# Kernel tuning notes

Measured on AMD Instinct MI355X. Metric: run time of the kernel, lower is better.

The kernel has to match this reference:

```python
import jax, jax.numpy as jnp
import numpy as np

EMBED_DIM = 1024
NUM_HEADS = 4
HEAD_DIM = EMBED_DIM // NUM_HEADS  # 256
QKV_DIM = 64                        # NUM_HEADS * QKV_DIM == HEAD_DIM (required by the residual add)
B, S = 16, 4096


def setup_inputs() -> dict:
    key = jax.random.key(0)
    kx, kq, kk, kv = jax.random.split(key, 4)
    x = jax.random.normal(kx, (B, S, EMBED_DIM), dtype=jnp.float32)
    # torch nn.Linear weights have shape [out_features, in_features]; y = x @ W.T
    scale = 1.0 / np.sqrt(HEAD_DIM)
    W_q = jax.random.normal(kq, (QKV_DIM, HEAD_DIM), dtype=jnp.float32) * scale
    W_k = jax.random.normal(kk, (QKV_DIM, HEAD_DIM), dtype=jnp.float32) * scale
    W_v = jax.random.normal(kv, (QKV_DIM, HEAD_DIM), dtype=jnp.float32) * scale
    return {"x": x, "W_q": W_q, "W_k": W_k, "W_v": W_v}


def reference(x, W_q, W_k, W_v):
    b = x.shape[0]
    # [B, S, H, Dh] -> [B, H, S, Dh]
    xh = x.reshape(b, -1, NUM_HEADS, HEAD_DIM).transpose(0, 2, 1, 3)
    # Shared projections applied per head (vectorized over the head axis)
    Q = jnp.einsum('bhsd,qd->bhsq', xh, W_q)  # [B,H,S,Qk]
    K = jnp.einsum('bhsd,qd->bhsq', xh, W_k)
    V = jnp.einsum('bhsd,qd->bhsq', xh, W_v)
    # Nonstandard ordering from the original: scores = Q^T K over the sequence axis
    attn_scores = jnp.einsum('bhsq,bhsk->bhqk', Q, K) / np.sqrt(HEAD_DIM)  # [B,H,Qk,Qk]
    attn_weights = jax.nn.softmax(attn_scores, axis=-1)
    # attn_output is computed in the original but NOT used in the returned value
    attn_output = jnp.einsum('bhsq,bhqk->bhsk', V, attn_weights)  # dead code, DCE'd under jit
    del attn_output
    # cat(V per head, dim=-1) -> [B, S, H*Qk];  x_head is the LAST head's slice [B, S, Dh]
    V_cat = V.transpose(0, 2, 1, 3).reshape(b, -1, NUM_HEADS * QKV_DIM)
    x_last_head = xh[:, NUM_HEADS - 1]  # [B, S, Dh]
    return x_last_head + V_cat
```

## Files before the change

kernel.cpp:

```cpp
#include <hip/hip_runtime.h>
#include <hip/hip_bf16.h>


#define TOKENS_PER_BLOCK 128
#define NCHUNK 8
#define NBLOCKS (16 * 4096 / TOKENS_PER_BLOCK)

typedef short bf16x4 __attribute__((ext_vector_type(4)));
typedef short bf16x8 __attribute__((ext_vector_type(8)));
typedef float f32x4  __attribute__((ext_vector_type(4)));

__device__ __forceinline__ short f2bf(float f) {
    __hip_bfloat16 h = __float2bfloat16(f);
    return __builtin_bit_cast(short, h);
}
__device__ __forceinline__ bf16x4 cvt4(f32x4 a) {
    bf16x4 r;
    r[0] = f2bf(a[0]); r[1] = f2bf(a[1]); r[2] = f2bf(a[2]); r[3] = f2bf(a[3]);
    return r;
}
__device__ __forceinline__ bf16x8 cvt8(f32x4 a, f32x4 b) {
    bf16x8 r;
    r[0] = f2bf(a[0]); r[1] = f2bf(a[1]); r[2] = f2bf(a[2]); r[3] = f2bf(a[3]);
    r[4] = f2bf(b[0]); r[5] = f2bf(b[1]); r[6] = f2bf(b[2]); r[7] = f2bf(b[3]);
    return r;
}

__device__ __forceinline__ int xofs(int tok, int colbyte) {
    return tok * 2048 + (colbyte ^ ((tok & 7) << 4));
}

__global__ __launch_bounds__(256, 1) void mha_vcat_kernel(
    const float* __restrict__ x, const float* __restrict__ Wv,
    float* __restrict__ out)
{
    __shared__ char X[2][16 * 2048];

    const int tid  = threadIdx.x;
    const int wid  = tid >> 6;
    const int lane = tid & 63;
    const int cl   = lane & 15;
    const int g    = lane >> 4;

    const long blockTok = (long)blockIdx.x * TOKENS_PER_BLOCK;

    const int srow  = tid >> 7;
    const int scolA = (tid & 127) * 4;

    f32x4 sA[8], sB[8];
    #pragma unroll
    for (int p = 0; p < 8; ++p) {
        const float* q = x + (blockTok + p * 2 + srow) * 1024;
        sA[p] = *(const f32x4*)(q + scolA);
        sB[p] = *(const f32x4*)(q + 512 + scolA);
    }

    bf16x8 wfr[8][4];
    #pragma unroll
    for (int kk = 0; kk < 8; ++kk)
        #pragma unroll
        for (int n = 0; n < 4; ++n) {
            const float* q = Wv + (n * 16 + cl) * 256 + kk * 32 + g * 8;
            wfr[kk][n] = cvt8(*(const f32x4*)q, *(const f32x4*)(q + 4));
        }

    bf16x8 diag0, diag1;
    #pragma unroll
    for (int j = 0; j < 8; ++j) {
        diag0[j] = (g * 8 + j == cl)      ? f2bf(1.0f) : (short)0;
        diag1[j] = (g * 8 + j == cl + 16) ? f2bf(1.0f) : (short)0;
    }

    #pragma unroll
    for (int p = 0; p < 8; ++p) {
        const int lt = p * 2 + srow;
        *(bf16x4*)(&X[0][xofs(lt, scolA * 2)])        = cvt4(sA[p]);
        *(bf16x4*)(&X[0][xofs(lt, 1024 + scolA * 2)]) = cvt4(sB[p]);
    }
    __syncthreads();

    #pragma unroll
    for (int c = 0; c < NCHUNK; ++c) {
        if (c < NCHUNK - 1) {
            #pragma unroll
            for (int p = 0; p < 8; ++p) {
                const float* q = x + (blockTok + (c + 1) * 16 + p * 2 + srow) * 1024;
                sA[p] = *(const f32x4*)(q + scolA);
                sB[p] = *(const f32x4*)(q + 512 + scolA);
            }
        }

        const char* Xb = X[c & 1];
        f32x4 acc[4];
        #pragma unroll
        for (int n = 0; n < 4; ++n) acc[n] = (f32x4){0.f, 0.f, 0.f, 0.f};

        #pragma unroll
        for (int kk = 0; kk < 8; ++kk) {
            const bf16x8 xf = *(const bf16x8*)(
                Xb + xofs(cl, wid * 512 + kk * 64 + g * 16));
            #pragma unroll
            for (int n = 0; n < 4; ++n)
                acc[n] = __builtin_amdgcn_mfma_f32_16x16x32_bf16(
                    wfr[kk][n], xf, acc[n], 0, 0, 0);
        }
        #pragma unroll
        for (int s = 0; s < 2; ++s) {
            const bf16x8 x3 = *(const bf16x8*)(
                Xb + xofs(cl, 1536 + wid * 128 + s * 64 + g * 16));
            acc[2 * s]     = __builtin_amdgcn_mfma_f32_16x16x32_bf16(
                diag0, x3, acc[2 * s], 0, 0, 0);
            acc[2 * s + 1] = __builtin_amdgcn_mfma_f32_16x16x32_bf16(
                diag1, x3, acc[2 * s + 1], 0, 0, 0);
        }

        float* trow = out + (blockTok + c * 16 + cl) * 256 + wid * 64;
        #pragma unroll
        for (int n = 0; n < 4; ++n)
            *(f32x4*)(trow + n * 16 + g * 4) = acc[n];

        if (c < NCHUNK - 1) {
            __syncthreads();
            char* Xn = X[(c + 1) & 1];
            #pragma unroll
            for (int p = 0; p < 8; ++p) {
                const int lt = p * 2 + srow;
                *(bf16x4*)(&Xn[xofs(lt, scolA * 2)])        = cvt4(sA[p]);
                *(bf16x4*)(&Xn[xofs(lt, 1024 + scolA * 2)]) = cvt4(sB[p]);
            }
            __syncthreads();
        }
    }
}

extern "C" void kernel_launch(void* const* d_in, const int* in_sizes, int n_in,
                              void* d_out, int out_size, void* d_ws, size_t ws_size,
                              hipStream_t stream) {
    const float* x  = (const float*)d_in[0];
    const float* Wv = (const float*)d_in[3];
    float* out = (float*)d_out;
    mha_vcat_kernel<<<dim3(NBLOCKS), dim3(256), 0, stream>>>(x, Wv, out);
}
```

Baseline: 82.32 us.

## Stage fp32 x directly into LDS via global_load_lds and add residual in fp32

Replaces register-staged loads with bf16 conversion into double-buffered LDS by direct global-to-LDS DMA of fp32 rows into a single swizzled buffer. The fp32 tiles are converted to bf16 when read for the MFMA. The residual head slice is now added in fp32 from LDS instead of through identity-matrix MFMAs. Tokens per block are halved and launch bounds raised to two blocks per CU to recover overlap. The single buffer serializes load and compute within a block, so latency hiding relies on the second resident block.

Result: faster. 78.40 us (-4.8%).

```diff
diff --git a/kernel.cpp b/kernel.cpp
--- a/kernel.cpp
+++ b/kernel.cpp
@@ -2,22 +2,17 @@
 #include <hip/hip_bf16.h>
 
 
-#define TOKENS_PER_BLOCK 128
-#define NCHUNK 8
-#define NBLOCKS (16 * 4096 / TOKENS_PER_BLOCK)
+#define NTOK (16 * 4096)
+#define TPB  64
+#define NCH  4
+#define NBLK (NTOK / TPB)
 
-typedef short bf16x4 __attribute__((ext_vector_type(4)));
 typedef short bf16x8 __attribute__((ext_vector_type(8)));
 typedef float f32x4  __attribute__((ext_vector_type(4)));
 
 __device__ __forceinline__ short f2bf(float f) {
     __hip_bfloat16 h = __float2bfloat16(f);
     return __builtin_bit_cast(short, h);
-}
-__device__ __forceinline__ bf16x4 cvt4(f32x4 a) {
-    bf16x4 r;
-    r[0] = f2bf(a[0]); r[1] = f2bf(a[1]); r[2] = f2bf(a[2]); r[3] = f2bf(a[3]);
-    return r;
 }
 __device__ __forceinline__ bf16x8 cvt8(f32x4 a, f32x4 b) {
     bf16x8 r;
@@ -26,34 +21,36 @@
     return r;
 }
 
-__device__ __forceinline__ int xofs(int tok, int colbyte) {
-    return tok * 2048 + (colbyte ^ ((tok & 7) << 4));
-}
-
-__global__ __launch_bounds__(256, 1) void mha_vcat_kernel(
+__global__ __launch_bounds__(256, 2) void mha_vcat_kernel(
     const float* __restrict__ x, const float* __restrict__ Wv,
     float* __restrict__ out)
 {
-    __shared__ char X[2][16 * 2048];
+    __shared__ float Xf[16 * 1024];
 
     const int tid  = threadIdx.x;
-    const int wid  = tid >> 6;
+    const int w    = tid >> 6;
     const int lane = tid & 63;
     const int cl   = lane & 15;
     const int g    = lane >> 4;
 
-    const long blockTok = (long)blockIdx.x * TOKENS_PER_BLOCK;
+    const long blockTok = (long)blockIdx.x * TPB;
 
-    const int srow  = tid >> 7;
-    const int scolA = (tid & 127) * 4;
+    auto stage = [&](int c) {
+        #pragma unroll
+        for (int i = 0; i < 16; ++i) {
+            const int tok = w * 4 + (i >> 2);
+            const int q   = i & 3;
+            const char* gp = (const char*)x
+                + (blockTok + c * 16 + tok) * 4096 + q * 1024
+                + ((lane * 16) ^ ((tok & 7) << 4));
+            float* lp = &Xf[tok * 1024 + q * 256];
+            __builtin_amdgcn_global_load_lds(
+                (const __attribute__((address_space(1))) void*)gp,
+                (__attribute__((address_space(3))) void*)lp, 16, 0, 0);
+        }
+    };
 
-    f32x4 sA[8], sB[8];
-    #pragma unroll
-    for (int p = 0; p < 8; ++p) {
-        const float* q = x + (blockTok + p * 2 + srow) * 1024;
-        sA[p] = *(const f32x4*)(q + scolA);
-        sB[p] = *(const f32x4*)(q + 512 + scolA);
-    }
+    stage(0);
 
     bf16x8 wfr[8][4];
     #pragma unroll
@@ -64,72 +61,39 @@
             wfr[kk][n] = cvt8(*(const f32x4*)q, *(const f32x4*)(q + 4));
         }
 
-    bf16x8 diag0, diag1;
-    #pragma unroll
-    for (int j = 0; j < 8; ++j) {
-        diag0[j] = (g * 8 + j == cl)      ? f2bf(1.0f) : (short)0;
-        diag1[j] = (g * 8 + j == cl + 16) ? f2bf(1.0f) : (short)0;
-    }
+    const int swz = (cl & 7) << 4;
+    const char* myrow = (const char*)Xf + cl * 4096;
 
-    #pragma unroll
-    for (int p = 0; p < 8; ++p) {
-        const int lt = p * 2 + srow;
-        *(bf16x4*)(&X[0][xofs(lt, scolA * 2)])        = cvt4(sA[p]);
-        *(bf16x4*)(&X[0][xofs(lt, 1024 + scolA * 2)]) = cvt4(sB[p]);
-    }
-    __syncthreads();
+    for (int c = 0; c < NCH; ++c) {
+        __syncthreads();
 
-    #pragma unroll
-    for (int c = 0; c < NCHUNK; ++c) {
-        if (c < NCHUNK - 1) {
-            #pragma unroll
-            for (int p = 0; p < 8; ++p) {
-                const float* q = x + (blockTok + (c + 1) * 16 + p * 2 + srow) * 1024;
-                sA[p] = *(const f32x4*)(q + scolA);
-                sB[p] = *(const f32x4*)(q + 512 + scolA);
-            }
-        }
-
-        const char* Xb = X[c & 1];
         f32x4 acc[4];
         #pragma unroll
         for (int n = 0; n < 4; ++n) acc[n] = (f32x4){0.f, 0.f, 0.f, 0.f};
 
         #pragma unroll
         for (int kk = 0; kk < 8; ++kk) {
-            const bf16x8 xf = *(const bf16x8*)(
-                Xb + xofs(cl, wid * 512 + kk * 64 + g * 16));
+            const int b = w * 1024 + kk * 128 + g * 32;
+            const f32x4 lo = *(const f32x4*)(myrow + ((b)      ^ swz));
+            const f32x4 hi = *(const f32x4*)(myrow + ((b + 16) ^ swz));
+            const bf16x8 xf = cvt8(lo, hi);
             #pragma unroll
             for (int n = 0; n < 4; ++n)
                 acc[n] = __builtin_amdgcn_mfma_f32_16x16x32_bf16(
                     wfr[kk][n], xf, acc[n], 0, 0, 0);
         }
+
+        float* trow = out + (blockTok + c * 16 + cl) * 256 + w * 64;
         #pragma unroll
-        for (int s = 0; s < 2; ++s) {
-            const bf16x8 x3 = *(const bf16x8*)(
-                Xb + xofs(cl, 1536 + wid * 128 + s * 64 + g * 16));
-            acc[2 * s]     = __builtin_amdgcn_mfma_f32_16x16x32_bf16(
-                diag0, x3, acc[2 * s], 0, 0, 0);
-            acc[2 * s + 1] = __builtin_amdgcn_mfma_f32_16x16x32_bf16(
-                diag1, x3, acc[2 * s + 1], 0, 0, 0);
+        for (int n = 0; n < 4; ++n) {
+            const int rb = 3072 + w * 256 + n * 64 + g * 16;
+            const f32x4 r = *(const f32x4*)(myrow + (rb ^ swz));
+            acc[n] += r;
+            *(f32x4*)(trow + n * 16 + g * 4) = acc[n];
         }
 
-        float* trow = out + (blockTok + c * 16 + cl) * 256 + wid * 64;
-        #pragma unroll
-        for (int n = 0; n < 4; ++n)
-            *(f32x4*)(trow + n * 16 + g * 4) = acc[n];
-
-        if (c < NCHUNK - 1) {
-            __syncthreads();
-            char* Xn = X[(c + 1) & 1];
-            #pragma unroll
-            for (int p = 0; p < 8; ++p) {
-                const int lt = p * 2 + srow;
-                *(bf16x4*)(&Xn[xofs(lt, scolA * 2)])        = cvt4(sA[p]);
-                *(bf16x4*)(&Xn[xofs(lt, 1024 + scolA * 2)]) = cvt4(sB[p]);
-            }
-            __syncthreads();
-        }
+        __syncthreads();
+        if (c + 1 < NCH) stage(c + 1);
     }
 }
 
@@ -139,5 +103,5 @@
     const float* x  = (const float*)d_in[0];
     const float* Wv = (const float*)d_in[3];
     float* out = (float*)d_out;
-    mha_vcat_kernel<<<dim3(NBLOCKS), dim3(256), 0, stream>>>(x, Wv, out);
+    mha_vcat_kernel<<<dim3(NBLK), dim3(256), 0, stream>>>(x, Wv, out);
 }
```
